# Performance work log

Measured on AMD Instinct MI355X. Metric: run time of the kernel, lower is better.

Reference implementation:

```python
import jax, jax.numpy as jnp
import numpy as np

NTOKEN = 64          # vocabulary size
MAX_PREFIX_LEN = 4   # tree depth D
D_MODEL = 648        # >= NTOKEN*(2*D+2) + D + 1 = 645


def setup_inputs() -> dict:
    key = jax.random.key(0)
    S, B = 2048, 8
    src = jax.random.randint(key, (S, B), 0, NTOKEN, dtype=jnp.int32)
    return {"src": src}


def _forward(src):
    n, D, d_model = NTOKEN, MAX_PREFIX_LEN, D_MODEL
    S, B = src.shape
    f32 = jnp.float32
    # shifted[k][t, b] = src[t-k, b] if t >= k else -1.
    # The -1 sentinel reproduces the all-zero one-hot rows the torch code creates
    # by zeroing extended_one_hot[0:i, :, ntoken*i].
    shifted = [src] + [
        jnp.concatenate([jnp.full((k, B), -1, src.dtype), src[: S - k]], axis=0)
        for k in range(1, D + 1)
    ]
    # one-hot blocks for offsets 0..D (sentinel -1 -> all-zero row)
    tok_ids = jnp.arange(n, dtype=src.dtype)
    onehots = [(s[..., None] == tok_ids).astype(f32) for s in shifted]  # each [S,B,n]
    one_hot0 = onehots[0]

    mask = jnp.tril(jnp.ones((S, S), f32), k=-1)  # mask[q, j] = 1 iff j < q

    # Incremental depth-i prefix match: at depth i the torch code compares
    # j_part block m (offset m+1, row j) against i_part block m (offset m, row q)
    # for m = 0..i-1; one-hot vectors are equal iff both tokens equal or both
    # out-of-range, which the sentinel encoding captures exactly.
    match = jnp.ones((S, S, B), bool)
    avg_blocks, count_chans = [], []
    for i in range(1, D + 1):
        match = match & (shifted[i - 1][:, None, :] == shifted[i][None, :, :])
        masked = match.astype(f32) * mask[:, :, None]            # [S(q), S(j), B]
        sums = jnp.einsum('qjb,jbt->qbt', masked, one_hot0)      # matched next-token one-hot sums
        counts = masked.sum(axis=1)[..., None]                   # [S, B, 1]
        avg_blocks.append(sums / jnp.clip(counts, 1))
        count_chans.append(counts)

    # Unconditional causal average over all j < q (exclusive prefix mean)
    cs = jnp.cumsum(one_hot0, axis=0)
    excl = jnp.concatenate([jnp.zeros((1, B, n), f32), cs[:-1]], axis=0)
    q_counts = jnp.broadcast_to(jnp.arange(S, dtype=f32)[:, None, None], (S, B, 1))
    avg_u = excl / jnp.clip(q_counts, 1)

    used = n * (2 * D + 2) + D + 1
    pad = jnp.zeros((S, B, d_model - used), f32)
    # channel layout (matches torch scatter/slice positions exactly):
    #   [0 .. n*(D+1))           one-hot blocks, offsets 0..D
    #   [n*(D+1) .. n*(2D+1))    depth-i matched averages, i=1..D
    #   [n*(2D+1) .. n*(2D+2))   unconditional causal average
    #   n*(2D+2)+i-1             depth-i match counts, i=1..D
    #   n*(2D+2)+D               unconditional count (= q)
    parts = onehots + avg_blocks + [avg_u] + count_chans + [q_counts, pad]
    return jnp.concatenate(parts, axis=-1)


def reference(src):
    return _forward(src)
```

## Files before the change

kernel.cpp:

```cpp
#include <hip/hip_runtime.h>

typedef unsigned long long u64;

#define S_LEN 2048
#define BATCH 8
#define NTOK 64
#define DMODEL 648
#define NBLK 32


__global__ __launch_bounds__(64) void build_kernel(const int* __restrict__ src,
                                                   u64* __restrict__ P,
                                                   u64* __restrict__ SH,
                                                   int* __restrict__ sT) {
    const int w = blockIdx.x, b = blockIdx.y;
    const int lane = threadIdx.x;
    const int p = (w << 6) + lane;
    const int tok  = src[p * BATCH + b];
    const int tokp = (w > 0) ? src[(p - 64) * BATCH + b] : -1;
    u64 m_sel = 0, mp_sel = 0;
    #pragma unroll 8
    for (int t = 0; t < NTOK; ++t) {
        const u64 m  = __ballot(tok == t);
        const u64 mp = __ballot(tokp == t);
        if (lane == t) { m_sel = m; mp_sel = mp; }
    }
    const int idx = (w << 6) + lane;
    P[b * 2048 + idx] = m_sel;
    u64* S = SH + (size_t)b * 8192;
    S[0 * 2048 + idx] = (m_sel << 1) | (mp_sel >> 63);
    S[1 * 2048 + idx] = (m_sel << 2) | (mp_sel >> 62);
    S[2 * 2048 + idx] = (m_sel << 3) | (mp_sel >> 61);
    S[3 * 2048 + idx] = (m_sel << 4) | (mp_sel >> 60);
    sT[b * S_LEN + p] = tok;
}

__global__ __launch_bounds__(256, 2) void compute_kernel(const u64* __restrict__ P,
                                                         const u64* __restrict__ SH,
                                                         const int* __restrict__ sT,
                                                         float* __restrict__ out) {
    __shared__ u64 L[4 * 2048];

    const int b = blockIdx.y;
    const int tid = threadIdx.x;
    const int lane = tid & 63;
    const int wv = tid >> 6;

    {
        const ulonglong2* G = (const ulonglong2*)(SH + (size_t)b * 8192);
        ulonglong2* Ld = (ulonglong2*)L;
        #pragma unroll 4
        for (int i = tid; i < 4096; i += 256) Ld[i] = G[i];
    }
    __syncthreads();

    const int o = blockIdx.x * 4 + wv;
    const int qoct = (o & 1) ? (255 - (o >> 1)) : (o >> 1);
    const int q0 = qoct << 3;

    const int* s = sT + b * S_LEN;
    const u64* Pb = P + (size_t)b * 2048;

    int tk[12];
    #pragma unroll
    for (int i = 0; i < 12; ++i) {
        const int idx = q0 - 4 + i;
        tk[i] = (idx >= 0) ? s[idx] : 0;
    }

    int hh[8][4] = {};
    int cuP[8];
    int cuF = 0;
    const int wq = q0 >> 6, rem0 = q0 & 63;

    u64 pv = Pb[lane];
    for (int w = 0; w < wq; ++w) {
        const u64 pvn = Pb[((w + 1) << 6) + lane];
        cuF += __popcll(pv);
        const int wb = w << 6;
        #pragma unroll
        for (int r = 0; r < 8; ++r) {
            const u64 A1 = L[wb + tk[4 + r]] & pv;
            const u64 A2 = A1 & L[2048 + wb + tk[3 + r]];
            const u64 A3 = A2 & L[4096 + wb + tk[2 + r]];
            const u64 A4 = A3 & L[6144 + wb + tk[1 + r]];
            hh[r][0] += __popcll(A1);
            hh[r][1] += __popcll(A2);
            hh[r][2] += __popcll(A3);
            hh[r][3] += __popcll(A4);
        }
        pv = pvn;
    }

    {
        const int wb = wq << 6;
        #pragma unroll
        for (int r = 0; r < 8; ++r) {
            const int rem = rem0 + r;
            const u64 valid = (1ull << rem) - 1ull;
            const u64 pvv = pv & valid;
            cuP[r] = cuF + __popcll(pvv);
            const u64 A1 = L[wb + tk[4 + r]] & pvv;
            const u64 A2 = A1 & L[2048 + wb + tk[3 + r]];
            const u64 A3 = A2 & L[4096 + wb + tk[2 + r]];
            const u64 A4 = A3 & L[6144 + wb + tk[1 + r]];
            hh[r][0] += __popcll(A1);
            hh[r][1] += __popcll(A2);
            hh[r][2] += __popcll(A3);
            hh[r][3] += __popcll(A4);
        }
    }

    #pragma unroll
    for (int r = 0; r < 8; ++r) {
        const int q = q0 + r;
        int p01 = hh[r][0] | (hh[r][1] << 16);
        int p23 = hh[r][2] | (hh[r][3] << 16);
        #pragma unroll
        for (int sft = 1; sft < 64; sft <<= 1) {
            p01 += __shfl_xor(p01, sft);
            p23 += __shfl_xor(p23, sft);
        }
        const int c1 = p01 & 0xffff, c2 = p01 >> 16;
        const int c3 = p23 & 0xffff, c4 = p23 >> 16;

        float* op = out + ((size_t)q * BATCH + b) * DMODEL;
        #pragma unroll
        for (int m = 0; m <= 4; ++m) {
            const bool sent = (q0 + r - m) < 0;
            op[m * 64 + lane] = (!sent && lane == tk[4 + r - m]) ? 1.f : 0.f;
        }
        op[320 + lane] = (float)hh[r][0] / (float)(c1 ? c1 : 1);
        op[384 + lane] = (float)hh[r][1] / (float)(c2 ? c2 : 1);
        op[448 + lane] = (float)hh[r][2] / (float)(c3 ? c3 : 1);
        op[512 + lane] = (float)hh[r][3] / (float)(c4 ? c4 : 1);
        op[576 + lane] = (float)cuP[r] / (float)(q ? q : 1);
        if (lane < 8) {
            float v = 0.f;
            if (lane == 0) v = (float)c1;
            else if (lane == 1) v = (float)c2;
            else if (lane == 2) v = (float)c3;
            else if (lane == 3) v = (float)c4;
            else if (lane == 4) v = (float)q;
            op[640 + lane] = v;
        }
    }
}

extern "C" void kernel_launch(void* const* d_in, const int* in_sizes, int n_in,
                              void* d_out, int out_size, void* d_ws, size_t ws_size,
                              hipStream_t stream) {
    const int* src = (const int*)d_in[0];
    float* out = (float*)d_out;
    u64* P  = (u64*)d_ws;
    u64* SH = P + 16384;
    int* sT = (int*)(P + 81920);

    build_kernel<<<dim3(NBLK, BATCH), 64, 0, stream>>>(src, P, SH, sT);
    compute_kernel<<<dim3(64, BATCH), 256, 0, stream>>>(P, SH, sT, out);
}
```

Baseline: 95.97 us.

## Fuse bitmask build into compute kernel with shared-memory atomics and reduced tables

Removes the separate build kernel and its global workspace: each block builds the per-window token bitmasks for its batch in shared memory with atomicOr, then derives shifted tables locally. Shift tables are cut from four to fewer arrays (depth-4 mask reconstructed from LS3 with a one-bit shift, depth-1/2 tables interleaved for 128-bit loads), lowering LDS footprint and allowing better occupancy. Each wave now handles two 4-row groups (balanced front/back) instead of one 8-row group, lowering register pressure. Costs: every one of the 64 blocks per batch redundantly rebuilds the tables, and more LDS loads per inner iteration.

```diff
diff --git a/kernel.cpp b/kernel.cpp
--- a/kernel.cpp
+++ b/kernel.cpp
@@ -4,145 +4,153 @@
 
 #define S_LEN 2048
 #define BATCH 8
-#define NTOK 64
 #define DMODEL 648
-#define NBLK 32
 
-
-__global__ __launch_bounds__(64) void build_kernel(const int* __restrict__ src,
-                                                   u64* __restrict__ P,
-                                                   u64* __restrict__ SH,
-                                                   int* __restrict__ sT) {
-    const int w = blockIdx.x, b = blockIdx.y;
-    const int lane = threadIdx.x;
-    const int p = (w << 6) + lane;
-    const int tok  = src[p * BATCH + b];
-    const int tokp = (w > 0) ? src[(p - 64) * BATCH + b] : -1;
-    u64 m_sel = 0, mp_sel = 0;
-    #pragma unroll 8
-    for (int t = 0; t < NTOK; ++t) {
-        const u64 m  = __ballot(tok == t);
-        const u64 mp = __ballot(tokp == t);
-        if (lane == t) { m_sel = m; mp_sel = mp; }
-    }
-    const int idx = (w << 6) + lane;
-    P[b * 2048 + idx] = m_sel;
-    u64* S = SH + (size_t)b * 8192;
-    S[0 * 2048 + idx] = (m_sel << 1) | (mp_sel >> 63);
-    S[1 * 2048 + idx] = (m_sel << 2) | (mp_sel >> 62);
-    S[2 * 2048 + idx] = (m_sel << 3) | (mp_sel >> 61);
-    S[3 * 2048 + idx] = (m_sel << 4) | (mp_sel >> 60);
-    sT[b * S_LEN + p] = tok;
-}
-
-__global__ __launch_bounds__(256, 2) void compute_kernel(const u64* __restrict__ P,
-                                                         const u64* __restrict__ SH,
-                                                         const int* __restrict__ sT,
-                                                         float* __restrict__ out) {
-    __shared__ u64 L[4 * 2048];
+__global__ __launch_bounds__(256, 2) void fused_kernel(const int* __restrict__ src,
+                                                       float* __restrict__ out) {
+    __shared__ __align__(16) u64 C1[2 * 2048];
+    __shared__ u64 LP[2048];
+    __shared__ u64 LS3[2048];
 
     const int b = blockIdx.y;
     const int tid = threadIdx.x;
     const int lane = tid & 63;
     const int wv = tid >> 6;
 
-    {
-        const ulonglong2* G = (const ulonglong2*)(SH + (size_t)b * 8192);
-        ulonglong2* Ld = (ulonglong2*)L;
-        #pragma unroll 4
-        for (int i = tid; i < 4096; i += 256) Ld[i] = G[i];
+    int myt[8];
+    #pragma unroll
+    for (int k = 0; k < 8; ++k) {
+        const int i = tid + 256 * k;
+        myt[k] = src[i * BATCH + b];
+        LP[i] = 0;
+    }
+    __syncthreads();
+    #pragma unroll
+    for (int k = 0; k < 8; ++k) {
+        const int i = tid + 256 * k;
+        atomicOr(&LP[(i & ~63) | myt[k]], 1ull << (i & 63));
+    }
+    __syncthreads();
+    #pragma unroll
+    for (int k = 0; k < 8; ++k) {
+        const int i = tid + 256 * k;
+        const u64 m = LP[i];
+        const u64 mp = (i >= 64) ? LP[i - 64] : 0ull;
+        C1[2 * i]     = (m << 1) | (mp >> 63);
+        C1[2 * i + 1] = (m << 2) | (mp >> 62);
+        LS3[i]        = (m << 3) | (mp >> 61);
     }
     __syncthreads();
 
     const int o = blockIdx.x * 4 + wv;
-    const int qoct = (o & 1) ? (255 - (o >> 1)) : (o >> 1);
-    const int q0 = qoct << 3;
 
-    const int* s = sT + b * S_LEN;
-    const u64* Pb = P + (size_t)b * 2048;
+    #pragma unroll 1
+    for (int half = 0; half < 2; ++half) {
+        const int quart = half ? (511 - o) : o;
+        const int q0 = quart << 2;
 
-    int tk[12];
-    #pragma unroll
-    for (int i = 0; i < 12; ++i) {
-        const int idx = q0 - 4 + i;
-        tk[i] = (idx >= 0) ? s[idx] : 0;
-    }
+        int tk[8];
+        #pragma unroll
+        for (int i = 0; i < 8; ++i) {
+            const int idx = q0 - 4 + i;
+            tk[i] = (idx >= 0) ? src[idx * BATCH + b] : 0;
+        }
 
-    int hh[8][4] = {};
-    int cuP[8];
-    int cuF = 0;
-    const int wq = q0 >> 6, rem0 = q0 & 63;
+        int h1[4] = {}, h2[4] = {}, h3[4] = {}, h4[4] = {};
+        int cuP[4];
+        int cuF = 0;
+        const int wq = q0 >> 6, rem0 = q0 & 63;
 
-    u64 pv = Pb[lane];
-    for (int w = 0; w < wq; ++w) {
-        const u64 pvn = Pb[((w + 1) << 6) + lane];
-        cuF += __popcll(pv);
-        const int wb = w << 6;
+        for (int w = 0; w < wq; ++w) {
+            const int wb = w << 6;
+            const int pb = w ? (wb - 64) : 0;
+            const u64 pv = LP[wb + lane];
+            cuF += __popcll(pv);
+            ulonglong2 pc = *(const ulonglong2*)&C1[2 * (wb + tk[3])];
+            u64 p3c = LS3[wb + tk[1]];
+            u64 p3p = w ? LS3[pb + tk[1]] : 0ull;
+            #pragma unroll
+            for (int r = 0; r < 4; ++r) {
+                const ulonglong2 c = *(const ulonglong2*)&C1[2 * (wb + tk[4 + r])];
+                const u64 s3c = LS3[wb + tk[2 + r]];
+                const u64 s3p = w ? LS3[pb + tk[2 + r]] : 0ull;
+                const u64 A1 = c.x & pv;
+                const u64 A2 = A1 & pc.y;
+                const u64 A3 = A2 & s3c;
+                const u64 A4 = A3 & ((p3c << 1) | (p3p >> 63));
+                h1[r] += __popcll(A1);
+                h2[r] += __popcll(A2);
+                h3[r] += __popcll(A3);
+                h4[r] += __popcll(A4);
+                pc = c; p3c = s3c; p3p = s3p;
+            }
+        }
+
+        {
+            const int wb = wq << 6;
+            const int pb = wq ? (wb - 64) : 0;
+            const u64 pv = LP[wb + lane];
+            ulonglong2 pc = *(const ulonglong2*)&C1[2 * (wb + tk[3])];
+            u64 p3c = LS3[wb + tk[1]];
+            u64 p3p = wq ? LS3[pb + tk[1]] : 0ull;
+            #pragma unroll
+            for (int r = 0; r < 4; ++r) {
+                const int rem = rem0 + r;
+                const u64 valid = (1ull << rem) - 1ull;
+                const u64 pvv = pv & valid;
+                cuP[r] = cuF + __popcll(pvv);
+                const ulonglong2 c = *(const ulonglong2*)&C1[2 * (wb + tk[4 + r])];
+                const u64 s3c = LS3[wb + tk[2 + r]];
+                const u64 s3p = wq ? LS3[pb + tk[2 + r]] : 0ull;
+                const u64 A1 = c.x & pvv;
+                const u64 A2 = A1 & pc.y;
+                const u64 A3 = A2 & s3c;
+                const u64 A4 = A3 & ((p3c << 1) | (p3p >> 63));
+                h1[r] += __popcll(A1);
+                h2[r] += __popcll(A2);
+                h3[r] += __popcll(A3);
+                h4[r] += __popcll(A4);
+                pc = c; p3c = s3c; p3p = s3p;
+            }
+        }
+
+        int c1v[4], c2v[4], c3v[4], c4v[4];
         #pragma unroll
-        for (int r = 0; r < 8; ++r) {
-            const u64 A1 = L[wb + tk[4 + r]] & pv;
-            const u64 A2 = A1 & L[2048 + wb + tk[3 + r]];
-            const u64 A3 = A2 & L[4096 + wb + tk[2 + r]];
-            const u64 A4 = A3 & L[6144 + wb + tk[1 + r]];
-            hh[r][0] += __popcll(A1);
-            hh[r][1] += __popcll(A2);
-            hh[r][2] += __popcll(A3);
-            hh[r][3] += __popcll(A4);
+        for (int r = 0; r < 4; ++r) {
+            int p01 = h1[r] | (h2[r] << 16);
+            int p23 = h3[r] | (h4[r] << 16);
+            #pragma unroll
+            for (int sft = 1; sft < 64; sft <<= 1) {
+                p01 += __shfl_xor(p01, sft);
+                p23 += __shfl_xor(p23, sft);
+            }
+            c1v[r] = p01 & 0xffff; c2v[r] = p01 >> 16;
+            c3v[r] = p23 & 0xffff; c4v[r] = p23 >> 16;
         }
-        pv = pvn;
-    }
 
-    {
-        const int wb = wq << 6;
         #pragma unroll
-        for (int r = 0; r < 8; ++r) {
-            const int rem = rem0 + r;
-            const u64 valid = (1ull << rem) - 1ull;
-            const u64 pvv = pv & valid;
-            cuP[r] = cuF + __popcll(pvv);
-            const u64 A1 = L[wb + tk[4 + r]] & pvv;
-            const u64 A2 = A1 & L[2048 + wb + tk[3 + r]];
-            const u64 A3 = A2 & L[4096 + wb + tk[2 + r]];
-            const u64 A4 = A3 & L[6144 + wb + tk[1 + r]];
-            hh[r][0] += __popcll(A1);
-            hh[r][1] += __popcll(A2);
-            hh[r][2] += __popcll(A3);
-            hh[r][3] += __popcll(A4);
-        }
-    }
-
-    #pragma unroll
-    for (int r = 0; r < 8; ++r) {
-        const int q = q0 + r;
-        int p01 = hh[r][0] | (hh[r][1] << 16);
-        int p23 = hh[r][2] | (hh[r][3] << 16);
-        #pragma unroll
-        for (int sft = 1; sft < 64; sft <<= 1) {
-            p01 += __shfl_xor(p01, sft);
-            p23 += __shfl_xor(p23, sft);
-        }
-        const int c1 = p01 & 0xffff, c2 = p01 >> 16;
-        const int c3 = p23 & 0xffff, c4 = p23 >> 16;
-
-        float* op = out + ((size_t)q * BATCH + b) * DMODEL;
-        #pragma unroll
-        for (int m = 0; m <= 4; ++m) {
-            const bool sent = (q0 + r - m) < 0;
-            op[m * 64 + lane] = (!sent && lane == tk[4 + r - m]) ? 1.f : 0.f;
-        }
-        op[320 + lane] = (float)hh[r][0] / (float)(c1 ? c1 : 1);
-        op[384 + lane] = (float)hh[r][1] / (float)(c2 ? c2 : 1);
-        op[448 + lane] = (float)hh[r][2] / (float)(c3 ? c3 : 1);
-        op[512 + lane] = (float)hh[r][3] / (float)(c4 ? c4 : 1);
-        op[576 + lane] = (float)cuP[r] / (float)(q ? q : 1);
-        if (lane < 8) {
-            float v = 0.f;
-            if (lane == 0) v = (float)c1;
-            else if (lane == 1) v = (float)c2;
-            else if (lane == 2) v = (float)c3;
-            else if (lane == 3) v = (float)c4;
-            else if (lane == 4) v = (float)q;
-            op[640 + lane] = v;
+        for (int r = 0; r < 4; ++r) {
+            const int q = q0 + r;
+            float* op = out + ((size_t)q * BATCH + b) * DMODEL;
+            #pragma unroll
+            for (int m = 0; m <= 4; ++m) {
+                const bool sent = (q - m) < 0;
+                op[m * 64 + lane] = (!sent && lane == tk[4 + r - m]) ? 1.f : 0.f;
+            }
+            op[320 + lane] = (float)h1[r] / (float)(c1v[r] ? c1v[r] : 1);
+            op[384 + lane] = (float)h2[r] / (float)(c2v[r] ? c2v[r] : 1);
+            op[448 + lane] = (float)h3[r] / (float)(c3v[r] ? c3v[r] : 1);
+            op[512 + lane] = (float)h4[r] / (float)(c4v[r] ? c4v[r] : 1);
+            op[576 + lane] = (float)cuP[r] / (float)(q ? q : 1);
+            if (lane < 8) {
+                float v = 0.f;
+                if (lane == 0) v = (float)c1v[r];
+                else if (lane == 1) v = (float)c2v[r];
+                else if (lane == 2) v = (float)c3v[r];
+                else if (lane == 3) v = (float)c4v[r];
+                else if (lane == 4) v = (float)q;
+                op[640 + lane] = v;
+            }
         }
     }
 }
@@ -152,10 +160,5 @@
                               hipStream_t stream) {
     const int* src = (const int*)d_in[0];
     float* out = (float*)d_out;
-    u64* P  = (u64*)d_ws;
-    u64* SH = P + 16384;
-    int* sT = (int*)(P + 81920);
-
-    build_kernel<<<dim3(NBLK, BATCH), 64, 0, stream>>>(src, P, SH, sT);
-    compute_kernel<<<dim3(64, BATCH), 256, 0, stream>>>(P, SH, sT, out);
+    fused_kernel<<<dim3(64, BATCH), 256, 0, stream>>>(src, out);
 }
```

Measured after the change: 84.50 us. 1.14x faster.

## Drop LDS staging and split queries into pairs across more blocks

Applied to the files above, without the earlier changes.

The compute kernel no longer copies the 64KB shifted-bitmask table into shared memory. It reads those masks directly from global memory, relying on L1/L2 caching. Each wave now handles two balanced pairs of query rows (a front pair and its mirrored back pair) instead of one octet, and the grid doubles to 128x8 blocks. The aim is to remove the LDS fill and its occupancy limit and to expose more parallelism. The cost is more redundant global reads of P and SH per query row, with less reuse per load.

```diff
diff --git a/kernel.cpp b/kernel.cpp
--- a/kernel.cpp
+++ b/kernel.cpp
@@ -35,114 +35,111 @@
     sT[b * S_LEN + p] = tok;
 }
 
-__global__ __launch_bounds__(256, 2) void compute_kernel(const u64* __restrict__ P,
-                                                         const u64* __restrict__ SH,
-                                                         const int* __restrict__ sT,
-                                                         float* __restrict__ out) {
-    __shared__ u64 L[4 * 2048];
-
+__global__ __launch_bounds__(256) void compute_kernel(const u64* __restrict__ P,
+                                                      const u64* __restrict__ SH,
+                                                      const int* __restrict__ sT,
+                                                      float* __restrict__ out) {
     const int b = blockIdx.y;
     const int tid = threadIdx.x;
     const int lane = tid & 63;
     const int wv = tid >> 6;
 
-    {
-        const ulonglong2* G = (const ulonglong2*)(SH + (size_t)b * 8192);
-        ulonglong2* Ld = (ulonglong2*)L;
-        #pragma unroll 4
-        for (int i = tid; i < 4096; i += 256) Ld[i] = G[i];
-    }
-    __syncthreads();
-
-    const int o = blockIdx.x * 4 + wv;
-    const int qoct = (o & 1) ? (255 - (o >> 1)) : (o >> 1);
-    const int q0 = qoct << 3;
+    const int k = blockIdx.x * 4 + wv;
 
     const int* s = sT + b * S_LEN;
     const u64* Pb = P + (size_t)b * 2048;
+    const u64* S1 = SH + (size_t)b * 8192;
+    const u64* S2 = S1 + 2048;
+    const u64* S3 = S1 + 4096;
+    const u64* S4 = S1 + 6144;
 
-    int tk[12];
-    #pragma unroll
-    for (int i = 0; i < 12; ++i) {
-        const int idx = q0 - 4 + i;
-        tk[i] = (idx >= 0) ? s[idx] : 0;
-    }
+    #pragma unroll 1
+    for (int g = 0; g < 2; ++g) {
+        const int pairid = g ? (1023 - k) : k;
+        const int q0 = pairid << 1;
 
-    int hh[8][4] = {};
-    int cuP[8];
-    int cuF = 0;
-    const int wq = q0 >> 6, rem0 = q0 & 63;
+        int tk[6];
+        #pragma unroll
+        for (int i = 0; i < 6; ++i) {
+            const int idx = q0 - 4 + i;
+            tk[i] = (idx >= 0) ? s[idx] : 0;
+        }
 
-    u64 pv = Pb[lane];
-    for (int w = 0; w < wq; ++w) {
-        const u64 pvn = Pb[((w + 1) << 6) + lane];
-        cuF += __popcll(pv);
-        const int wb = w << 6;
+        int h1[2] = {}, h2[2] = {}, h3[2] = {}, h4[2] = {};
+        int cuP[2];
+        int cuF = 0;
+        const int wq = q0 >> 6, rem0 = q0 & 63;
+
+        for (int w = 0; w < wq; ++w) {
+            const int wb = w << 6;
+            const u64 pv = Pb[wb + lane];
+            cuF += __popcll(pv);
+            #pragma unroll
+            for (int r = 0; r < 2; ++r) {
+                const u64 A1 = S1[wb + tk[4 + r]] & pv;
+                const u64 A2 = A1 & S2[wb + tk[3 + r]];
+                const u64 A3 = A2 & S3[wb + tk[2 + r]];
+                const u64 A4 = A3 & S4[wb + tk[1 + r]];
+                h1[r] += __popcll(A1);
+                h2[r] += __popcll(A2);
+                h3[r] += __popcll(A3);
+                h4[r] += __popcll(A4);
+            }
+        }
+
+        {
+            const int wb = wq << 6;
+            const u64 pv = Pb[wb + lane];
+            #pragma unroll
+            for (int r = 0; r < 2; ++r) {
+                const int rem = rem0 + r;
+                const u64 valid = (1ull << rem) - 1ull;
+                const u64 pvv = pv & valid;
+                cuP[r] = cuF + __popcll(pvv);
+                const u64 A1 = S1[wb + tk[4 + r]] & pvv;
+                const u64 A2 = A1 & S2[wb + tk[3 + r]];
+                const u64 A3 = A2 & S3[wb + tk[2 + r]];
+                const u64 A4 = A3 & S4[wb + tk[1 + r]];
+                h1[r] += __popcll(A1);
+                h2[r] += __popcll(A2);
+                h3[r] += __popcll(A3);
+                h4[r] += __popcll(A4);
+            }
+        }
+
         #pragma unroll
-        for (int r = 0; r < 8; ++r) {
-            const u64 A1 = L[wb + tk[4 + r]] & pv;
-            const u64 A2 = A1 & L[2048 + wb + tk[3 + r]];
-            const u64 A3 = A2 & L[4096 + wb + tk[2 + r]];
-            const u64 A4 = A3 & L[6144 + wb + tk[1 + r]];
-            hh[r][0] += __popcll(A1);
-            hh[r][1] += __popcll(A2);
-            hh[r][2] += __popcll(A3);
-            hh[r][3] += __popcll(A4);
-        }
-        pv = pvn;
-    }
+        for (int r = 0; r < 2; ++r) {
+            const int q = q0 + r;
+            int p01 = h1[r] | (h2[r] << 16);
+            int p23 = h3[r] | (h4[r] << 16);
+            #pragma unroll
+            for (int sft = 1; sft < 64; sft <<= 1) {
+                p01 += __shfl_xor(p01, sft);
+                p23 += __shfl_xor(p23, sft);
+            }
+            const int c1 = p01 & 0xffff, c2 = p01 >> 16;
+            const int c3 = p23 & 0xffff, c4 = p23 >> 16;
 
-    {
-        const int wb = wq << 6;
-        #pragma unroll
-        for (int r = 0; r < 8; ++r) {
-            const int rem = rem0 + r;
-            const u64 valid = (1ull << rem) - 1ull;
-            const u64 pvv = pv & valid;
-            cuP[r] = cuF + __popcll(pvv);
-            const u64 A1 = L[wb + tk[4 + r]] & pvv;
-            const u64 A2 = A1 & L[2048 + wb + tk[3 + r]];
-            const u64 A3 = A2 & L[4096 + wb + tk[2 + r]];
-            const u64 A4 = A3 & L[6144 + wb + tk[1 + r]];
-            hh[r][0] += __popcll(A1);
-            hh[r][1] += __popcll(A2);
-            hh[r][2] += __popcll(A3);
-            hh[r][3] += __popcll(A4);
-        }
-    }
-
-    #pragma unroll
-    for (int r = 0; r < 8; ++r) {
-        const int q = q0 + r;
-        int p01 = hh[r][0] | (hh[r][1] << 16);
-        int p23 = hh[r][2] | (hh[r][3] << 16);
-        #pragma unroll
-        for (int sft = 1; sft < 64; sft <<= 1) {
-            p01 += __shfl_xor(p01, sft);
-            p23 += __shfl_xor(p23, sft);
-        }
-        const int c1 = p01 & 0xffff, c2 = p01 >> 16;
-        const int c3 = p23 & 0xffff, c4 = p23 >> 16;
-
-        float* op = out + ((size_t)q * BATCH + b) * DMODEL;
-        #pragma unroll
-        for (int m = 0; m <= 4; ++m) {
-            const bool sent = (q0 + r - m) < 0;
-            op[m * 64 + lane] = (!sent && lane == tk[4 + r - m]) ? 1.f : 0.f;
-        }
-        op[320 + lane] = (float)hh[r][0] / (float)(c1 ? c1 : 1);
-        op[384 + lane] = (float)hh[r][1] / (float)(c2 ? c2 : 1);
-        op[448 + lane] = (float)hh[r][2] / (float)(c3 ? c3 : 1);
-        op[512 + lane] = (float)hh[r][3] / (float)(c4 ? c4 : 1);
-        op[576 + lane] = (float)cuP[r] / (float)(q ? q : 1);
-        if (lane < 8) {
-            float v = 0.f;
-            if (lane == 0) v = (float)c1;
-            else if (lane == 1) v = (float)c2;
-            else if (lane == 2) v = (float)c3;
-            else if (lane == 3) v = (float)c4;
-            else if (lane == 4) v = (float)q;
-            op[640 + lane] = v;
+            float* op = out + ((size_t)q * BATCH + b) * DMODEL;
+            #pragma unroll
+            for (int m = 0; m <= 4; ++m) {
+                const bool sent = (q - m) < 0;
+                op[m * 64 + lane] = (!sent && lane == tk[4 + r - m]) ? 1.f : 0.f;
+            }
+            op[320 + lane] = (float)h1[r] / (float)(c1 ? c1 : 1);
+            op[384 + lane] = (float)h2[r] / (float)(c2 ? c2 : 1);
+            op[448 + lane] = (float)h3[r] / (float)(c3 ? c3 : 1);
+            op[512 + lane] = (float)h4[r] / (float)(c4 ? c4 : 1);
+            op[576 + lane] = (float)cuP[r] / (float)(q ? q : 1);
+            if (lane < 8) {
+                float v = 0.f;
+                if (lane == 0) v = (float)c1;
+                else if (lane == 1) v = (float)c2;
+                else if (lane == 2) v = (float)c3;
+                else if (lane == 3) v = (float)c4;
+                else if (lane == 4) v = (float)q;
+                op[640 + lane] = v;
+            }
         }
     }
 }
@@ -157,5 +154,5 @@
     int* sT = (int*)(P + 81920);
 
     build_kernel<<<dim3(NBLK, BATCH), 64, 0, stream>>>(src, P, SH, sT);
-    compute_kernel<<<dim3(64, BATCH), 256, 0, stream>>>(P, SH, sT, out);
+    compute_kernel<<<dim3(128, BATCH), 256, 0, stream>>>(P, SH, sT, out);
 }
```

Measured after the change: 105.2 us. +9.7%, slower.
